# Performance work log

Measured on AMD Instinct MI355X. Metric: run time of the kernel, lower is better.

The kernel has to match this reference:

```python
import jax, jax.numpy as jnp
import numpy as np

D_MODEL = 1024
ADAPT = 128
NUM_LIB = 8
BATCH = 1024


def setup_inputs() -> dict:
    key = jax.random.key(0)
    k_x, k_src, k_tgt, k_w1, k_w2 = jax.random.split(key, 5)
    hidden_states = jax.random.normal(k_x, (BATCH, D_MODEL), dtype=jnp.float32)
    source_library = jax.random.randint(k_src, (BATCH,), 0, NUM_LIB, dtype=jnp.int32)
    target_library = jax.random.randint(k_tgt, (BATCH,), 0, NUM_LIB, dtype=jnp.int32)
    # Stacked translator weights: slot p = src*NUM_LIB + tgt. Diagonal slots
    # (src==tgt) exist for uniform indexing but are masked out (identity path).
    P = NUM_LIB * NUM_LIB
    s1 = 1.0 / np.sqrt(D_MODEL).astype(np.float32)
    s2 = 1.0 / np.sqrt(ADAPT).astype(np.float32)
    W1 = jax.random.normal(k_w1, (P, D_MODEL, ADAPT), dtype=jnp.float32) * s1
    b1 = jnp.zeros((P, ADAPT), dtype=jnp.float32)
    W2 = jax.random.normal(k_w2, (P, ADAPT, D_MODEL), dtype=jnp.float32) * s2
    b2 = jnp.zeros((P, D_MODEL), dtype=jnp.float32)
    return {
        "hidden_states": hidden_states,
        "source_library": source_library,
        "target_library": target_library,
        "W1": W1, "b1": b1, "W2": W2, "b2": b2,
    }


def reference(hidden_states, source_library, target_library, W1, b1, W2, b2):
    # L recovered from stacked expert table [L*L, d, a]
    L = int(np.sqrt(W1.shape[0]))
    pair = source_library * L + target_library  # [B]
    # Per-sample expert weights (grouped-GEMM formulation of the python loop)
    h = jax.nn.relu(jnp.einsum('bd,bda->ba', hidden_states, W1[pair]) + b1[pair])
    y = jnp.einsum('ba,bad->bd', h, W2[pair]) + b2[pair]
    # src == tgt -> identity (original appends hidden_states[i] unchanged)
    same = (source_library == target_library)[:, None]
    return jnp.where(same, hidden_states, y)
```

## Files before the change

### kernel.cpp

```cpp
#include <hip/hip_runtime.h>
#include <hip/hip_bf16.h>

#define D_MODEL 1024
#define ADAPT   128
#define NUM_LIB 8
#define BATCH   1024
#define CH      32

typedef __attribute__((ext_vector_type(8))) short bf16x8;
typedef __attribute__((ext_vector_type(4))) float f32x4;

__device__ __forceinline__ unsigned pk2(float a, float b) {
  __hip_bfloat162 h = __float22bfloat162_rn(make_float2(a, b));
  return *(unsigned*)&h;
}

#define BK     256
#define XS_STR 264
#define WT_STR 264

__global__ __launch_bounds__(256) void gemm1_k(const float* __restrict__ x,
                                               const float* __restrict__ W1,
                                               const int* __restrict__ src,
                                               const int* __restrict__ tgt,
                                               float* __restrict__ Hp) {
  int p = blockIdx.x;
  if ((p % 9) == 0) return;
  int a0 = blockIdx.y * 64;
  int k0 = blockIdx.z * BK;
  __shared__ int   nrows;
  __shared__ int   rows_l[BATCH];
  __shared__ short xs[CH * XS_STR];
  __shared__ short wt[64 * WT_STR];
  int t = threadIdx.x;
  if (t == 0) nrows = 0;
  __syncthreads();
  {
#pragma unroll
    for (int i = 0; i < 4; i++) {
      int s = t + 256 * i;
      int pr = src[s] * NUM_LIB + tgt[s];
      if (pr == p) rows_l[atomicAdd(&nrows, 1)] = s;
    }
  }
  {
    int a_st = t & 63, kg = t >> 6;
    const float* wr = W1 + ((size_t)p * D_MODEL + k0 + kg * 64) * ADAPT + a0 + a_st;
    uint4* ww = (uint4*)(wt + a_st * WT_STR + kg * 64);
#pragma unroll
    for (int j8 = 0; j8 < 8; j8++) {
      uint4 o;
      o.x = pk2(wr[(j8 * 8 + 0) * ADAPT], wr[(j8 * 8 + 1) * ADAPT]);
      o.y = pk2(wr[(j8 * 8 + 2) * ADAPT], wr[(j8 * 8 + 3) * ADAPT]);
      o.z = pk2(wr[(j8 * 8 + 4) * ADAPT], wr[(j8 * 8 + 5) * ADAPT]);
      o.w = pk2(wr[(j8 * 8 + 6) * ADAPT], wr[(j8 * 8 + 7) * ADAPT]);
      ww[j8] = o;
    }
  }
  __syncthreads();
  int n = nrows;
  if (n == 0) return;
  int lane = t & 63, wvid = t >> 6, col = lane & 15, quad = lane >> 4;
  float* Hb = Hp + (size_t)blockIdx.z * BATCH * ADAPT;
  for (int c0 = 0; c0 < n; c0 += CH) {
    int m = min(CH, n - c0);
    {
      int s = t & 31, jg = t >> 5;
      int row = rows_l[c0 + min(s, m - 1)];
      const float* xr = x + (size_t)row * D_MODEL + k0 + jg * 32;
      uint4* xw = (uint4*)(xs + s * XS_STR + jg * 32);
#pragma unroll
      for (int i = 0; i < 4; i++) {
        float4 v0 = *(const float4*)(xr + i * 8);
        float4 v1 = *(const float4*)(xr + i * 8 + 4);
        uint4 o;
        o.x = pk2(v0.x, v0.y); o.y = pk2(v0.z, v0.w);
        o.z = pk2(v1.x, v1.y); o.w = pk2(v1.z, v1.w);
        xw[i] = o;
      }
    }
    __syncthreads();
    f32x4 acc0 = {0.f, 0.f, 0.f, 0.f};
    f32x4 acc1 = {0.f, 0.f, 0.f, 0.f};
#pragma unroll
    for (int kk = 0; kk < 8; kk++) {
      bf16x8 af0 = *(const bf16x8*)(xs + col * XS_STR + kk * 32 + quad * 8);
      bf16x8 af1 = *(const bf16x8*)(xs + (16 + col) * XS_STR + kk * 32 + quad * 8);
      bf16x8 bv  = *(const bf16x8*)(wt + (wvid * 16 + col) * WT_STR + kk * 32 + quad * 8);
      acc0 = __builtin_amdgcn_mfma_f32_16x16x32_bf16(af0, bv, acc0, 0, 0, 0);
      acc1 = __builtin_amdgcn_mfma_f32_16x16x32_bf16(af1, bv, acc1, 0, 0, 0);
    }
    int a = a0 + wvid * 16 + col;
#pragma unroll
    for (int r = 0; r < 4; r++) {
      int s2 = quad * 4 + r;
      if (s2 < m)      Hb[(size_t)rows_l[c0 + s2] * ADAPT + a]      = acc0[r];
      if (s2 + 16 < m) Hb[(size_t)rows_l[c0 + s2 + 16] * ADAPT + a] = acc1[r];
    }
    if (c0 + CH < n) __syncthreads();
  }
}

#define HS_STR  136
#define WT2_STR 136

__global__ __launch_bounds__(256) void gemm2_k(const float* __restrict__ x,
                                               const float* __restrict__ W2,
                                               const float* __restrict__ b1,
                                               const float* __restrict__ b2,
                                               const int* __restrict__ src,
                                               const int* __restrict__ tgt,
                                               const float* __restrict__ Hp,
                                               float* __restrict__ out) {
  int p = blockIdx.x;
  int d0 = blockIdx.y * 128;
  __shared__ int nrows;
  __shared__ int rows_l[BATCH];
  int t = threadIdx.x;
  if (t == 0) nrows = 0;
  __syncthreads();
  {
#pragma unroll
    for (int i = 0; i < 4; i++) {
      int s = t + 256 * i;
      int pr = src[s] * NUM_LIB + tgt[s];
      if (pr == p) rows_l[atomicAdd(&nrows, 1)] = s;
    }
  }
  if ((p % 9) == 0) {
    __syncthreads();
    int n = nrows;
    int j = t & 7;
    for (int c = t >> 3; c < n; c += 32) {
      size_t off = (size_t)rows_l[c] * D_MODEL + d0 + j * 16;
      float4 v0 = *(const float4*)(x + off);
      float4 v1 = *(const float4*)(x + off + 4);
      float4 v2 = *(const float4*)(x + off + 8);
      float4 v3 = *(const float4*)(x + off + 12);
      *(float4*)(out + off)      = v0;
      *(float4*)(out + off + 4)  = v1;
      *(float4*)(out + off + 8)  = v2;
      *(float4*)(out + off + 12) = v3;
    }
    return;
  }
  __shared__ short hs[CH * HS_STR];
  __shared__ short wt[128 * WT2_STR];
  {
    int dl = t & 127, half = t >> 7;
#pragma unroll
    for (int kgi = 0; kgi < 8; kgi++) {
      int kb = kgi * 16 + half * 8;
      const float* wr = W2 + ((size_t)p * ADAPT + kb) * D_MODEL + d0 + dl;
      uint4 o;
      o.x = pk2(wr[0 * D_MODEL], wr[1 * D_MODEL]);
      o.y = pk2(wr[2 * D_MODEL], wr[3 * D_MODEL]);
      o.z = pk2(wr[4 * D_MODEL], wr[5 * D_MODEL]);
      o.w = pk2(wr[6 * D_MODEL], wr[7 * D_MODEL]);
      *(uint4*)(wt + dl * WT2_STR + kb) = o;
    }
  }
  __syncthreads();
  int n = nrows;
  if (n == 0) return;
  int lane = t & 63, wvid = t >> 6, col = lane & 15, quad = lane >> 4;
  for (int c0 = 0; c0 < n; c0 += CH) {
    int m = min(CH, n - c0);
    {
      int s = t & 31, j = t >> 5;
      int row = rows_l[c0 + min(s, m - 1)];
      size_t ho = (size_t)row * ADAPT + j * 16;
      const float* bb = b1 + (size_t)p * ADAPT + j * 16;
      uint4* hw = (uint4*)(hs + s * HS_STR + j * 16);
#pragma unroll
      for (int g = 0; g < 2; g++) {
        float v[8];
#pragma unroll
        for (int i = 0; i < 8; i++) {
          float acc = bb[g * 8 + i];
#pragma unroll
          for (int q = 0; q < 4; q++) acc += Hp[(size_t)q * BATCH * ADAPT + ho + g * 8 + i];
          v[i] = fmaxf(acc, 0.f);
        }
        uint4 o;
        o.x = pk2(v[0], v[1]); o.y = pk2(v[2], v[3]);
        o.z = pk2(v[4], v[5]); o.w = pk2(v[6], v[7]);
        hw[g] = o;
      }
    }
    __syncthreads();
    f32x4 acc00 = {0.f, 0.f, 0.f, 0.f};
    f32x4 acc01 = {0.f, 0.f, 0.f, 0.f};
    f32x4 acc10 = {0.f, 0.f, 0.f, 0.f};
    f32x4 acc11 = {0.f, 0.f, 0.f, 0.f};
#pragma unroll
    for (int kk = 0; kk < 4; kk++) {
      bf16x8 af0 = *(const bf16x8*)(hs + col * HS_STR + kk * 32 + quad * 8);
      bf16x8 af1 = *(const bf16x8*)(hs + (16 + col) * HS_STR + kk * 32 + quad * 8);
      bf16x8 b0  = *(const bf16x8*)(wt + (wvid * 32 + col) * WT2_STR + kk * 32 + quad * 8);
      bf16x8 b1v = *(const bf16x8*)(wt + (wvid * 32 + 16 + col) * WT2_STR + kk * 32 + quad * 8);
      acc00 = __builtin_amdgcn_mfma_f32_16x16x32_bf16(af0, b0,  acc00, 0, 0, 0);
      acc01 = __builtin_amdgcn_mfma_f32_16x16x32_bf16(af0, b1v, acc01, 0, 0, 0);
      acc10 = __builtin_amdgcn_mfma_f32_16x16x32_bf16(af1, b0,  acc10, 0, 0, 0);
      acc11 = __builtin_amdgcn_mfma_f32_16x16x32_bf16(af1, b1v, acc11, 0, 0, 0);
    }
    int d_a = d0 + wvid * 32 + col;
    int d_b = d_a + 16;
    float bba = b2[(size_t)p * D_MODEL + d_a];
    float bbb = b2[(size_t)p * D_MODEL + d_b];
#pragma unroll
    for (int r = 0; r < 4; r++) {
      int s2 = quad * 4 + r;
      if (s2 < m) {
        size_t ro = (size_t)rows_l[c0 + s2] * D_MODEL;
        out[ro + d_a] = acc00[r] + bba;
        out[ro + d_b] = acc01[r] + bbb;
      }
      if (s2 + 16 < m) {
        size_t ro = (size_t)rows_l[c0 + s2 + 16] * D_MODEL;
        out[ro + d_a] = acc10[r] + bba;
        out[ro + d_b] = acc11[r] + bbb;
      }
    }
    if (c0 + CH < n) __syncthreads();
  }
}

extern "C" void kernel_launch(void* const* d_in, const int* in_sizes, int n_in,
                              void* d_out, int out_size, void* d_ws, size_t ws_size,
                              hipStream_t stream) {
  const float* x   = (const float*)d_in[0];
  const int*   src = (const int*)d_in[1];
  const int*   tgt = (const int*)d_in[2];
  const float* W1  = (const float*)d_in[3];
  const float* b1  = (const float*)d_in[4];
  const float* W2  = (const float*)d_in[5];
  const float* b2  = (const float*)d_in[6];
  float* out = (float*)d_out;

  float* Hp = (float*)d_ws;

  gemm1_k<<<dim3(64, 2, 4), 256, 0, stream>>>(x, W1, src, tgt, Hp);
  gemm2_k<<<dim3(64, 8), 256, 0, stream>>>(x, W2, b1, b2, src, tgt, Hp, out);
  (void)in_sizes; (void)n_in; (void)out_size; (void)ws_size;
}
```

Before: 117.2 us.

## Keep weight B-fragments in registers instead of LDS staging in both GEMMs

Both GEMM kernels now load their weight tile straight from global memory into per-lane registers in MFMA B-fragment layout, converting to bf16 in registers rather than writing a transposed tile to shared memory and reading it back. The weight loads are issued before the row-list atomics and barrier so their latency overlaps the routing scan. The second kernel also vectorizes the partial-sum reduction of Hp with float4 loads. This removes LDS traffic and the weight staging footprint, which may raise occupancy, at the cost of more registers per thread.

```diff
diff --git a/kernel.cpp b/kernel.cpp
--- a/kernel.cpp
+++ b/kernel.cpp
@@ -15,9 +15,15 @@
   return *(unsigned*)&h;
 }
 
+__device__ __forceinline__ bf16x8 pk8(const float* v) {
+  union { uint4 u; bf16x8 b; } o;
+  o.u.x = pk2(v[0], v[1]); o.u.y = pk2(v[2], v[3]);
+  o.u.z = pk2(v[4], v[5]); o.u.w = pk2(v[6], v[7]);
+  return o.b;
+}
+
 #define BK     256
 #define XS_STR 264
-#define WT_STR 264
 
 __global__ __launch_bounds__(256) void gemm1_k(const float* __restrict__ x,
                                                const float* __restrict__ W1,
@@ -31,36 +37,35 @@
   __shared__ int   nrows;
   __shared__ int   rows_l[BATCH];
   __shared__ short xs[CH * XS_STR];
-  __shared__ short wt[64 * WT_STR];
   int t = threadIdx.x;
   if (t == 0) nrows = 0;
   __syncthreads();
-  {
-#pragma unroll
-    for (int i = 0; i < 4; i++) {
-      int s = t + 256 * i;
-      int pr = src[s] * NUM_LIB + tgt[s];
-      if (pr == p) rows_l[atomicAdd(&nrows, 1)] = s;
-    }
-  }
-  {
-    int a_st = t & 63, kg = t >> 6;
-    const float* wr = W1 + ((size_t)p * D_MODEL + k0 + kg * 64) * ADAPT + a0 + a_st;
-    uint4* ww = (uint4*)(wt + a_st * WT_STR + kg * 64);
-#pragma unroll
-    for (int j8 = 0; j8 < 8; j8++) {
-      uint4 o;
-      o.x = pk2(wr[(j8 * 8 + 0) * ADAPT], wr[(j8 * 8 + 1) * ADAPT]);
-      o.y = pk2(wr[(j8 * 8 + 2) * ADAPT], wr[(j8 * 8 + 3) * ADAPT]);
-      o.z = pk2(wr[(j8 * 8 + 4) * ADAPT], wr[(j8 * 8 + 5) * ADAPT]);
-      o.w = pk2(wr[(j8 * 8 + 6) * ADAPT], wr[(j8 * 8 + 7) * ADAPT]);
-      ww[j8] = o;
-    }
-  }
+  int lane = t & 63, wvid = t >> 6, col = lane & 15, quad = lane >> 4;
+
+  int prv[4];
+#pragma unroll
+  for (int i = 0; i < 4; i++) {
+    int s = t + 256 * i;
+    prv[i] = src[s] * NUM_LIB + tgt[s];
+  }
+  int a = a0 + wvid * 16 + col;
+  const float* wb = W1 + ((size_t)p * D_MODEL + k0 + quad * 8) * ADAPT + a;
+  float wv[8][8];
+#pragma unroll
+  for (int kk = 0; kk < 8; kk++)
+#pragma unroll
+    for (int j = 0; j < 8; j++)
+      wv[kk][j] = wb[(kk * 32 + j) * ADAPT];
+#pragma unroll
+  for (int i = 0; i < 4; i++)
+    if (prv[i] == p) rows_l[atomicAdd(&nrows, 1)] = t + 256 * i;
   __syncthreads();
   int n = nrows;
   if (n == 0) return;
-  int lane = t & 63, wvid = t >> 6, col = lane & 15, quad = lane >> 4;
+  bf16x8 bfrag[8];
+#pragma unroll
+  for (int kk = 0; kk < 8; kk++) bfrag[kk] = pk8(wv[kk]);
+
   float* Hb = Hp + (size_t)blockIdx.z * BATCH * ADAPT;
   for (int c0 = 0; c0 < n; c0 += CH) {
     int m = min(CH, n - c0);
@@ -86,11 +91,9 @@
     for (int kk = 0; kk < 8; kk++) {
       bf16x8 af0 = *(const bf16x8*)(xs + col * XS_STR + kk * 32 + quad * 8);
       bf16x8 af1 = *(const bf16x8*)(xs + (16 + col) * XS_STR + kk * 32 + quad * 8);
-      bf16x8 bv  = *(const bf16x8*)(wt + (wvid * 16 + col) * WT_STR + kk * 32 + quad * 8);
-      acc0 = __builtin_amdgcn_mfma_f32_16x16x32_bf16(af0, bv, acc0, 0, 0, 0);
-      acc1 = __builtin_amdgcn_mfma_f32_16x16x32_bf16(af1, bv, acc1, 0, 0, 0);
-    }
-    int a = a0 + wvid * 16 + col;
+      acc0 = __builtin_amdgcn_mfma_f32_16x16x32_bf16(af0, bfrag[kk], acc0, 0, 0, 0);
+      acc1 = __builtin_amdgcn_mfma_f32_16x16x32_bf16(af1, bfrag[kk], acc1, 0, 0, 0);
+    }
 #pragma unroll
     for (int r = 0; r < 4; r++) {
       int s2 = quad * 4 + r;
@@ -102,7 +105,6 @@
 }
 
 #define HS_STR  136
-#define WT2_STR 136
 
 __global__ __launch_bounds__(256) void gemm2_k(const float* __restrict__ x,
                                                const float* __restrict__ W2,
@@ -114,20 +116,22 @@
                                                float* __restrict__ out) {
   int p = blockIdx.x;
   int d0 = blockIdx.y * 128;
-  __shared__ int nrows;
-  __shared__ int rows_l[BATCH];
+  __shared__ int   nrows;
+  __shared__ int   rows_l[BATCH];
+  __shared__ short hs[CH * HS_STR];
   int t = threadIdx.x;
   if (t == 0) nrows = 0;
   __syncthreads();
-  {
-#pragma unroll
-    for (int i = 0; i < 4; i++) {
-      int s = t + 256 * i;
-      int pr = src[s] * NUM_LIB + tgt[s];
-      if (pr == p) rows_l[atomicAdd(&nrows, 1)] = s;
-    }
+  int prv[4];
+#pragma unroll
+  for (int i = 0; i < 4; i++) {
+    int s = t + 256 * i;
+    prv[i] = src[s] * NUM_LIB + tgt[s];
   }
   if ((p % 9) == 0) {
+#pragma unroll
+    for (int i = 0; i < 4; i++)
+      if (prv[i] == p) rows_l[atomicAdd(&nrows, 1)] = t + 256 * i;
     __syncthreads();
     int n = nrows;
     int j = t & 7;
@@ -144,26 +148,28 @@
     }
     return;
   }
-  __shared__ short hs[CH * HS_STR];
-  __shared__ short wt[128 * WT2_STR];
-  {
-    int dl = t & 127, half = t >> 7;
-#pragma unroll
-    for (int kgi = 0; kgi < 8; kgi++) {
-      int kb = kgi * 16 + half * 8;
-      const float* wr = W2 + ((size_t)p * ADAPT + kb) * D_MODEL + d0 + dl;
-      uint4 o;
-      o.x = pk2(wr[0 * D_MODEL], wr[1 * D_MODEL]);
-      o.y = pk2(wr[2 * D_MODEL], wr[3 * D_MODEL]);
-      o.z = pk2(wr[4 * D_MODEL], wr[5 * D_MODEL]);
-      o.w = pk2(wr[6 * D_MODEL], wr[7 * D_MODEL]);
-      *(uint4*)(wt + dl * WT2_STR + kb) = o;
-    }
-  }
+  int lane = t & 63, wvid = t >> 6, col = lane & 15, quad = lane >> 4;
+  const float* w2b = W2 + ((size_t)p * ADAPT + quad * 8) * D_MODEL + d0 + wvid * 32 + col;
+  float wv[4][2][8];
+#pragma unroll
+  for (int kk = 0; kk < 4; kk++)
+#pragma unroll
+    for (int c = 0; c < 2; c++)
+#pragma unroll
+      for (int j = 0; j < 8; j++)
+        wv[kk][c][j] = w2b[(size_t)(kk * 32 + j) * D_MODEL + c * 16];
+#pragma unroll
+  for (int i = 0; i < 4; i++)
+    if (prv[i] == p) rows_l[atomicAdd(&nrows, 1)] = t + 256 * i;
   __syncthreads();
   int n = nrows;
   if (n == 0) return;
-  int lane = t & 63, wvid = t >> 6, col = lane & 15, quad = lane >> 4;
+  bf16x8 bfragB[4][2];
+#pragma unroll
+  for (int kk = 0; kk < 4; kk++) {
+    bfragB[kk][0] = pk8(wv[kk][0]);
+    bfragB[kk][1] = pk8(wv[kk][1]);
+  }
   for (int c0 = 0; c0 < n; c0 += CH) {
     int m = min(CH, n - c0);
     {
@@ -174,17 +180,19 @@
       uint4* hw = (uint4*)(hs + s * HS_STR + j * 16);
 #pragma unroll
       for (int g = 0; g < 2; g++) {
-        float v[8];
-#pragma unroll
-        for (int i = 0; i < 8; i++) {
-          float acc = bb[g * 8 + i];
-#pragma unroll
-          for (int q = 0; q < 4; q++) acc += Hp[(size_t)q * BATCH * ADAPT + ho + g * 8 + i];
-          v[i] = fmaxf(acc, 0.f);
+        f32x4 v0 = *(const f32x4*)(bb + g * 8);
+        f32x4 v1 = *(const f32x4*)(bb + g * 8 + 4);
+#pragma unroll
+        for (int q = 0; q < 4; q++) {
+          const float* hq = Hp + (size_t)q * BATCH * ADAPT + ho + g * 8;
+          v0 += *(const f32x4*)hq;
+          v1 += *(const f32x4*)(hq + 4);
         }
         uint4 o;
-        o.x = pk2(v[0], v[1]); o.y = pk2(v[2], v[3]);
-        o.z = pk2(v[4], v[5]); o.w = pk2(v[6], v[7]);
+        o.x = pk2(fmaxf(v0[0], 0.f), fmaxf(v0[1], 0.f));
+        o.y = pk2(fmaxf(v0[2], 0.f), fmaxf(v0[3], 0.f));
+        o.z = pk2(fmaxf(v1[0], 0.f), fmaxf(v1[1], 0.f));
+        o.w = pk2(fmaxf(v1[2], 0.f), fmaxf(v1[3], 0.f));
         hw[g] = o;
       }
     }
@@ -197,12 +205,10 @@
     for (int kk = 0; kk < 4; kk++) {
       bf16x8 af0 = *(const bf16x8*)(hs + col * HS_STR + kk * 32 + quad * 8);
       bf16x8 af1 = *(const bf16x8*)(hs + (16 + col) * HS_STR + kk * 32 + quad * 8);
-      bf16x8 b0  = *(const bf16x8*)(wt + (wvid * 32 + col) * WT2_STR + kk * 32 + quad * 8);
-      bf16x8 b1v = *(const bf16x8*)(wt + (wvid * 32 + 16 + col) * WT2_STR + kk * 32 + quad * 8);
-      acc00 = __builtin_amdgcn_mfma_f32_16x16x32_bf16(af0, b0,  acc00, 0, 0, 0);
-      acc01 = __builtin_amdgcn_mfma_f32_16x16x32_bf16(af0, b1v, acc01, 0, 0, 0);
-      acc10 = __builtin_amdgcn_mfma_f32_16x16x32_bf16(af1, b0,  acc10, 0, 0, 0);
-      acc11 = __builtin_amdgcn_mfma_f32_16x16x32_bf16(af1, b1v, acc11, 0, 0, 0);
+      acc00 = __builtin_amdgcn_mfma_f32_16x16x32_bf16(af0, bfragB[kk][0], acc00, 0, 0, 0);
+      acc01 = __builtin_amdgcn_mfma_f32_16x16x32_bf16(af0, bfragB[kk][1], acc01, 0, 0, 0);
+      acc10 = __builtin_amdgcn_mfma_f32_16x16x32_bf16(af1, bfragB[kk][0], acc10, 0, 0, 0);
+      acc11 = __builtin_amdgcn_mfma_f32_16x16x32_bf16(af1, bfragB[kk][1], acc11, 0, 0, 0);
     }
     int d_a = d0 + wvid * 32 + col;
     int d_b = d_a + 16;
```

New measurement: 116.8 us. Within noise of the previous version (-0.4%).
